# Performance work log

Hardware: AMD Instinct MI355X
Metric: run time of the kernel (lower is better)

## Reference

```python
import jax, jax.numpy as jnp
import numpy as np

B_SZ, L, H, P = 4, 4096, 1024, 1024
R_MIN, R_MAX, MAX_PHASE = 0.0, 1.0, 6.28


def setup_inputs() -> dict:
    key = jax.random.key(0)
    ks = jax.random.split(key, 8)
    inputs = jax.random.normal(ks[0], (B_SZ, L, H), dtype=jnp.float32)
    # LRU-style init for nu_log/theta_log (keeps |lambda| < 1 so scan is stable)
    u1 = jax.random.uniform(ks[1], (P,))
    nu = -0.5 * jnp.log(u1 * (R_MAX**2 - R_MIN**2) + R_MIN**2)
    nu_log = jnp.log(nu)
    u2 = jax.random.uniform(ks[2], (P,))
    theta_log = jnp.log(MAX_PHASE * u2)
    # variance_scaling(0.5,'fan_out','normal') for B; (1.0,'fan_out','normal') for C
    B_re = jax.random.normal(ks[3], (P, H)) * jnp.sqrt(0.5 / P)
    B_im = jax.random.normal(ks[4], (P, H)) * jnp.sqrt(0.5 / P)
    C_re = jax.random.normal(ks[5], (H, P)) * jnp.sqrt(1.0 / H)
    C_im = jax.random.normal(ks[6], (H, P)) * jnp.sqrt(1.0 / H)
    D = jax.random.normal(ks[7], (H,))
    diag_lambda = jnp.exp(-jnp.exp(nu_log) + 1j * jnp.exp(theta_log))
    gamma_log = jnp.log(jnp.sqrt(1.0 - jnp.abs(diag_lambda) ** 2))
    return {
        "inputs": inputs,
        "nu_log": nu_log.astype(jnp.float32),
        "theta_log": theta_log.astype(jnp.float32),
        "B_re": B_re.astype(jnp.float32),
        "B_im": B_im.astype(jnp.float32),
        "C_re": C_re.astype(jnp.float32),
        "C_im": C_im.astype(jnp.float32),
        "D": D.astype(jnp.float32),
        "gamma_log": gamma_log.astype(jnp.float32),
    }


def reference(inputs, nu_log, theta_log, B_re, B_im, C_re, C_im, D, gamma_log):
    batch_size, input_length, _ = inputs.shape
    Lambda = jnp.exp(-jnp.exp(nu_log) + 1j * jnp.exp(theta_log))  # [P] complex
    Bmat = B_re + 1j * B_im                                        # [P,H]
    Cmat = C_re + 1j * C_im                                        # [H,P]
    gamma = jnp.exp(gamma_log)                                     # [P]
    B_norm = Bmat * gamma[:, None]

    def apply_step(elem_i, elem_j):
        a_i, bu_i = elem_i
        a_j, bu_j = elem_j
        return (a_j * a_i, a_j * bu_i + bu_j)

    Ls = jnp.broadcast_to(Lambda, (batch_size, input_length, Lambda.shape[0]))
    Bu = jnp.einsum('ph,blh->blp', B_norm, inputs.astype(B_norm.dtype))
    _, xs = jax.lax.associative_scan(apply_step, (Ls, Bu), axis=1)
    Cx = jnp.einsum('hp,blp->blh', Cmat, xs).real
    Du = D * inputs
    return Cx + Du
```

## Files before the change

### kernel.cpp

```cpp
#include <hip/hip_runtime.h>
#include <cstdint>
#include <cstddef>

#define MDIM 16384
#define HDIM 1024
#define PDIM 1024
#define LSEQ 4096
#define BSZ  4
#define CHUNK 64
#define NCHUNK 64
#define NBU  2048

typedef float   floatx4  __attribute__((ext_vector_type(4)));
typedef __bf16  bf16x8   __attribute__((ext_vector_type(8)));
typedef unsigned short u16;
typedef unsigned short u16x8 __attribute__((ext_vector_type(8)));
typedef unsigned short u16x4 __attribute__((ext_vector_type(4)));

__device__ __forceinline__ u16 f2bf(float f) {
    union { float f; uint32_t u; } v; v.f = f;
    return (u16)((v.u + 0x7fffu + ((v.u >> 16) & 1u)) >> 16);
}
__device__ __forceinline__ float bfu2f(uint32_t bits16) {
    union { float f; uint32_t u; } v; v.u = bits16 << 16; return v.f;
}
__device__ __forceinline__ bf16x8 ldfrag(const u16* p) {
    return __builtin_bit_cast(bf16x8, *(const u16x8*)p);
}
__device__ __forceinline__ void gload16(const u16* g, u16* l) {
    __builtin_amdgcn_global_load_lds(
        (const __attribute__((address_space(1))) uint32_t*)g,
        (__attribute__((address_space(3))) uint32_t*)l, 16, 0, 0);
}

template<int KD>
__device__ __forceinline__ void gemm_core(
    const u16* __restrict__ A, const u16* __restrict__ B,
    int m0, int n0, u16* sA, u16* sB, floatx4 acc[4][4])
{
    const int tid  = threadIdx.x;
    const int wave = tid >> 6, lane = tid & 63;
    const int lrow = lane & 15, lq = lane >> 4;
    const int wm = (wave >> 1) * 64, wn = (wave & 1) * 64;
    const int srow   = lane >> 3;
    const int schunk = (lane & 7) ^ srow;

    const u16* aptr = A + (size_t)(m0 + wave * 32 + srow) * KD + schunk * 8;
    const u16* bptr = B + (size_t)(n0 + wave * 32 + srow) * KD + schunk * 8;
    u16* sAw = sA + wave * 32 * 64;
    u16* sBw = sB + wave * 32 * 64;

    for (int k0 = 0; k0 < KD; k0 += 64) {
        #pragma unroll
        for (int i = 0; i < 4; ++i) {
            gload16(aptr + (size_t)i * 8 * KD + k0, sAw + i * 8 * 64);
            gload16(bptr + (size_t)i * 8 * KD + k0, sBw + i * 8 * 64);
        }
        __syncthreads();
        #pragma unroll
        for (int s = 0; s < 2; ++s) {
            bf16x8 af[4], bfr[4];
            #pragma unroll
            for (int mt = 0; mt < 4; ++mt) {
                int r = wm + mt * 16 + lrow;
                af[mt] = ldfrag(sA + r * 64 + (((s * 4 + lq) ^ (r & 7)) * 8));
            }
            #pragma unroll
            for (int nt = 0; nt < 4; ++nt) {
                int r = wn + nt * 16 + lrow;
                bfr[nt] = ldfrag(sB + r * 64 + (((s * 4 + lq) ^ (r & 7)) * 8));
            }
            #pragma unroll
            for (int mt = 0; mt < 4; ++mt)
                #pragma unroll
                for (int nt = 0; nt < 4; ++nt)
                    acc[mt][nt] = __builtin_amdgcn_mfma_f32_16x16x32_bf16(
                        af[mt], bfr[nt], acc[mt][nt], 0, 0, 0);
        }
        __syncthreads();
    }
}

__global__ __launch_bounds__(256) void gemm_bu_k(
    const u16* __restrict__ A, const u16* __restrict__ B, u16* __restrict__ O)
{
    __shared__ u16 sA[128 * 64];
    __shared__ u16 sB[128 * 64];
    floatx4 acc[4][4] = {};
    const int m0 = blockIdx.x * 128, n0 = blockIdx.y * 128;
    gemm_core<HDIM>(A, B, m0, n0, sA, sB, acc);

    const int tid = threadIdx.x, wave = tid >> 6, lane = tid & 63;
    const int lrow = lane & 15, lq = lane >> 4;
    const int wm = (wave >> 1) * 64, wn = (wave & 1) * 64;
    #pragma unroll
    for (int nt = 0; nt < 4; ++nt) {
        int col = n0 + wn + nt * 16 + lrow;
        #pragma unroll
        for (int mt = 0; mt < 4; ++mt)
            #pragma unroll
            for (int r = 0; r < 4; ++r) {
                int row = m0 + wm + mt * 16 + lq * 4 + r;
                O[(size_t)row * NBU + col] = f2bf(acc[mt][nt][r]);
            }
    }
}

__global__ __launch_bounds__(256) void gemm_out_k(
    const u16* __restrict__ A, const u16* __restrict__ B,
    const float* __restrict__ Dv, const u16* __restrict__ Ubf,
    float* __restrict__ O)
{
    __shared__ u16 sA[128 * 64];
    __shared__ u16 sB[128 * 64];
    floatx4 acc[4][4] = {};
    const int m0 = blockIdx.x * 128, n0 = blockIdx.y * 128;
    gemm_core<NBU>(A, B, m0, n0, sA, sB, acc);

    const int tid = threadIdx.x, wave = tid >> 6, lane = tid & 63;
    const int lrow = lane & 15, lq = lane >> 4;
    const int wm = (wave >> 1) * 64, wn = (wave & 1) * 64;
    #pragma unroll
    for (int nt = 0; nt < 4; ++nt) {
        int col = n0 + wn + nt * 16 + lrow;
        float d = Dv[col];
        #pragma unroll
        for (int mt = 0; mt < 4; ++mt)
            #pragma unroll
            for (int r = 0; r < 4; ++r) {
                int row = m0 + wm + mt * 16 + lq * 4 + r;
                size_t o = (size_t)row * HDIM + col;
                O[o] = acc[mt][nt][r] + d * bfu2f(Ubf[o]);
            }
    }
}

__global__ __launch_bounds__(256) void cvt_u_bf(
    const float* __restrict__ in, u16* __restrict__ out)
{
    size_t i = ((size_t)blockIdx.x * 256 + threadIdx.x) * 8;
    float4 a = *(const float4*)(in + i);
    float4 b = *(const float4*)(in + i + 4);
    u16x8 w;
    w[0]=f2bf(a.x); w[1]=f2bf(a.y); w[2]=f2bf(a.z); w[3]=f2bf(a.w);
    w[4]=f2bf(b.x); w[5]=f2bf(b.y); w[6]=f2bf(b.z); w[7]=f2bf(b.w);
    *(u16x8*)(out + i) = w;
}

__global__ __launch_bounds__(256) void prep_bcomb(
    const float* __restrict__ Bre, const float* __restrict__ Bim,
    const float* __restrict__ gamma_log, u16* __restrict__ out)
{
    int t = blockIdx.x * 256 + threadIdx.x;
    int n = t >> 7;
    int h = (t & 127) * 8;
    int p = n >> 1, s = n & 1;
    const float* src = (s ? Bim : Bre) + (size_t)p * HDIM + h;
    float g = expf(gamma_log[p]);
    float4 a = *(const float4*)src;
    float4 b = *(const float4*)(src + 4);
    u16x8 w;
    w[0]=f2bf(a.x*g); w[1]=f2bf(a.y*g); w[2]=f2bf(a.z*g); w[3]=f2bf(a.w*g);
    w[4]=f2bf(b.x*g); w[5]=f2bf(b.y*g); w[6]=f2bf(b.z*g); w[7]=f2bf(b.w*g);
    *(u16x8*)(out + (size_t)n * HDIM + h) = w;
}

__global__ __launch_bounds__(256) void prep_bc(
    const float* __restrict__ Cre, const float* __restrict__ Cim,
    u16* __restrict__ out)
{
    int t = blockIdx.x * 256 + threadIdx.x;
    int h = t >> 8;
    int k = (t & 255) * 4;
    float4 cr = *(const float4*)(Cre + (size_t)h * PDIM + k);
    float4 ci = *(const float4*)(Cim + (size_t)h * PDIM + k);
    u16x8 w;
    w[0]=f2bf(cr.x); w[1]=f2bf(-ci.x);
    w[2]=f2bf(cr.y); w[3]=f2bf(-ci.y);
    w[4]=f2bf(cr.z); w[5]=f2bf(-ci.z);
    w[6]=f2bf(cr.w); w[7]=f2bf(-ci.w);
    *(u16x8*)(out + (size_t)h * NBU + 2 * k) = w;
}

__global__ __launch_bounds__(256) void scan_passA(
    const uint32_t* __restrict__ BuC,
    const float* __restrict__ nu_log, const float* __restrict__ theta_log,
    float* __restrict__ endC)
{
    int tid = blockIdx.x * 256 + threadIdx.x;
    int p = tid & (PDIM - 1);
    int c = (tid >> 10) & (NCHUNK - 1);
    int b = tid >> 16;
    float nu = expf(nu_log[p]);
    float th = expf(theta_log[p]);
    float el = expf(-nu);
    float lr = el * cosf(th), li = el * sinf(th);
    const uint32_t* src = BuC + (size_t)(b * LSEQ + c * CHUNK) * PDIM + p;
    float xr = 0.f, xi = 0.f;
    #pragma unroll 8
    for (int t = 0; t < CHUNK; ++t) {
        uint32_t v = src[(size_t)t * PDIM];
        float br = bfu2f(v & 0xffffu), bi = bfu2f(v >> 16);
        float nr = fmaf(lr, xr, fmaf(-li, xi, br));
        float ni = fmaf(lr, xi, fmaf(li, xr, bi));
        xr = nr; xi = ni;
    }
    float2 e; e.x = xr; e.y = xi;
    *(float2*)(endC + (size_t)tid * 2) = e;
}

__global__ __launch_bounds__(256) void scan_passB(
    const float* __restrict__ endC,
    const float* __restrict__ nu_log, const float* __restrict__ theta_log,
    float* __restrict__ carryC)
{
    int tid = blockIdx.x * 256 + threadIdx.x;
    int p = tid & (PDIM - 1);
    int b = tid >> 10;
    float nu = expf(nu_log[p]);
    float th = expf(theta_log[p]);
    float e64 = expf(-nu * (float)CHUNK);
    float a = th * (float)CHUNK;
    float Lr = e64 * cosf(a), Li = e64 * sinf(a);
    float gr = 0.f, gi = 0.f;
    for (int c = 0; c < NCHUNK; ++c) {
        size_t idx = (((size_t)b * NCHUNK + c) * PDIM + p) * 2;
        float2 g; g.x = gr; g.y = gi;
        *(float2*)(carryC + idx) = g;
        float2 e = *(const float2*)(endC + idx);
        float nr = fmaf(Lr, gr, fmaf(-Li, gi, e.x));
        float ni = fmaf(Lr, gi, fmaf(Li, gr, e.y));
        gr = nr; gi = ni;
    }
}

__global__ __launch_bounds__(256) void scan_passC(
    uint32_t* __restrict__ BuC,
    const float* __restrict__ nu_log, const float* __restrict__ theta_log,
    const float* __restrict__ carryC)
{
    int tid = blockIdx.x * 256 + threadIdx.x;
    int p = tid & (PDIM - 1);
    int c = (tid >> 10) & (NCHUNK - 1);
    int b = tid >> 16;
    float nu = expf(nu_log[p]);
    float th = expf(theta_log[p]);
    float el = expf(-nu);
    float lr = el * cosf(th), li = el * sinf(th);
    float2 g = *(const float2*)(carryC + (size_t)tid * 2);
    float xr = g.x, xi = g.y;
    uint32_t* ptr = BuC + (size_t)(b * LSEQ + c * CHUNK) * PDIM + p;
    #pragma unroll 8
    for (int t = 0; t < CHUNK; ++t) {
        uint32_t v = ptr[(size_t)t * PDIM];
        float br = bfu2f(v & 0xffffu), bi = bfu2f(v >> 16);
        float nr = fmaf(lr, xr, fmaf(-li, xi, br));
        float ni = fmaf(lr, xi, fmaf(li, xr, bi));
        xr = nr; xi = ni;
        ptr[(size_t)t * PDIM] = (uint32_t)f2bf(xr) | ((uint32_t)f2bf(xi) << 16);
    }
}

extern "C" void kernel_launch(void* const* d_in, const int* in_sizes, int n_in,
                              void* d_out, int out_size, void* d_ws, size_t ws_size,
                              hipStream_t stream)
{
    (void)in_sizes; (void)n_in; (void)out_size; (void)ws_size;
    const float* U         = (const float*)d_in[0];
    const float* nu_log    = (const float*)d_in[1];
    const float* theta_log = (const float*)d_in[2];
    const float* B_re      = (const float*)d_in[3];
    const float* B_im      = (const float*)d_in[4];
    const float* C_re      = (const float*)d_in[5];
    const float* C_im      = (const float*)d_in[6];
    const float* Dv        = (const float*)d_in[7];
    const float* gamma_log = (const float*)d_in[8];
    float* out = (float*)d_out;

    char* ws = (char*)d_ws;
    u16*      BuC    = (u16*)ws;
    u16*      Ubf    = (u16*)(ws + (size_t)64 * 1024 * 1024);
    u16*      Bcomb  = (u16*)(ws + (size_t)96 * 1024 * 1024);
    u16*      Bcbf   = (u16*)(ws + (size_t)100 * 1024 * 1024);
    float*    endC   = (float*)(ws + (size_t)104 * 1024 * 1024);
    float*    carryC = (float*)(ws + (size_t)106 * 1024 * 1024);

    cvt_u_bf <<<(MDIM * HDIM) / (256 * 8), 256, 0, stream>>>(U, Ubf);
    prep_bcomb<<<(NBU * HDIM) / (256 * 8), 256, 0, stream>>>(B_re, B_im, gamma_log, Bcomb);
    prep_bc  <<<(HDIM * PDIM) / (256 * 4), 256, 0, stream>>>(C_re, C_im, Bcbf);

    dim3 g1(MDIM / 128, NBU / 128);
    gemm_bu_k<<<g1, 256, 0, stream>>>(Ubf, Bcomb, BuC);

    const int nscan = BSZ * NCHUNK * PDIM;
    scan_passA<<<nscan / 256, 256, 0, stream>>>((const uint32_t*)BuC, nu_log, theta_log, endC);
    scan_passB<<<(BSZ * PDIM) / 256, 256, 0, stream>>>(endC, nu_log, theta_log, carryC);
    scan_passC<<<nscan / 256, 256, 0, stream>>>((uint32_t*)BuC, nu_log, theta_log, carryC);

    dim3 g3(MDIM / 128, HDIM / 128);
    gemm_out_k<<<g3, 256, 0, stream>>>(BuC, Bcbf, Dv, Ubf, out);
}
```

Before: 359.5 us.

## Stage GEMM output through LDS, swap grid order, and process two states per scan thread

The Bu GEMM epilogue now writes the bf16 tile to padded shared memory and stores it to global memory in 16-byte coalesced rows, replacing scattered 2-byte stores. Both GEMMs swap grid axes so consecutive blocks walk along N, which changes L2 reuse of the A tiles. All three scan passes handle two adjacent P states per thread with wider vector loads and stores, and pass B batches its endC loads eight at a time for more memory-level parallelism. The cost is half as many threads in the scan passes, which lowers the parallelism available for the sequential recurrences.

```diff
diff --git a/kernel.cpp b/kernel.cpp
--- a/kernel.cpp
+++ b/kernel.cpp
@@ -15,7 +15,6 @@
 typedef __bf16  bf16x8   __attribute__((ext_vector_type(8)));
 typedef unsigned short u16;
 typedef unsigned short u16x8 __attribute__((ext_vector_type(8)));
-typedef unsigned short u16x4 __attribute__((ext_vector_type(4)));
 
 __device__ __forceinline__ u16 f2bf(float f) {
     union { float f; uint32_t u; } v; v.f = f;
@@ -81,28 +80,41 @@
     }
 }
 
+#define ST 136
 __global__ __launch_bounds__(256) void gemm_bu_k(
     const u16* __restrict__ A, const u16* __restrict__ B, u16* __restrict__ O)
 {
-    __shared__ u16 sA[128 * 64];
-    __shared__ u16 sB[128 * 64];
+    __shared__ u16 smem[128 * ST];
+    u16* sA = smem;
+    u16* sB = smem + 128 * 64;
     floatx4 acc[4][4] = {};
-    const int m0 = blockIdx.x * 128, n0 = blockIdx.y * 128;
+    const int n0 = blockIdx.x * 128, m0 = blockIdx.y * 128;
     gemm_core<HDIM>(A, B, m0, n0, sA, sB, acc);
 
     const int tid = threadIdx.x, wave = tid >> 6, lane = tid & 63;
     const int lrow = lane & 15, lq = lane >> 4;
     const int wm = (wave >> 1) * 64, wn = (wave & 1) * 64;
+
     #pragma unroll
     for (int nt = 0; nt < 4; ++nt) {
-        int col = n0 + wn + nt * 16 + lrow;
+        int col = wn + nt * 16 + lrow;
         #pragma unroll
         for (int mt = 0; mt < 4; ++mt)
             #pragma unroll
             for (int r = 0; r < 4; ++r) {
-                int row = m0 + wm + mt * 16 + lq * 4 + r;
-                O[(size_t)row * NBU + col] = f2bf(acc[mt][nt][r]);
+                int row = wm + mt * 16 + lq * 4 + r;
+                smem[row * ST + col] = f2bf(acc[mt][nt][r]);
             }
+    }
+    __syncthreads();
+
+    const int col = (tid & 15) * 8;
+    const int rb  = tid >> 4;
+    #pragma unroll
+    for (int j = 0; j < 8; ++j) {
+        int row = rb + j * 16;
+        *(u16x8*)(O + (size_t)(m0 + row) * NBU + n0 + col) =
+            *(const u16x8*)(smem + row * ST + col);
     }
 }
 
@@ -114,7 +126,7 @@
     __shared__ u16 sA[128 * 64];
     __shared__ u16 sB[128 * 64];
     floatx4 acc[4][4] = {};
-    const int m0 = blockIdx.x * 128, n0 = blockIdx.y * 128;
+    const int n0 = blockIdx.x * 128, m0 = blockIdx.y * 128;
     gemm_core<NBU>(A, B, m0, n0, sA, sB, acc);
 
     const int tid = threadIdx.x, wave = tid >> 6, lane = tid & 63;
@@ -188,25 +200,29 @@
     float* __restrict__ endC)
 {
     int tid = blockIdx.x * 256 + threadIdx.x;
-    int p = tid & (PDIM - 1);
-    int c = (tid >> 10) & (NCHUNK - 1);
-    int b = tid >> 16;
-    float nu = expf(nu_log[p]);
-    float th = expf(theta_log[p]);
-    float el = expf(-nu);
-    float lr = el * cosf(th), li = el * sinf(th);
-    const uint32_t* src = BuC + (size_t)(b * LSEQ + c * CHUNK) * PDIM + p;
-    float xr = 0.f, xi = 0.f;
+    int p0 = (tid & 511) * 2;
+    int c  = (tid >> 9) & (NCHUNK - 1);
+    int b  = tid >> 15;
+    float nu0 = expf(nu_log[p0]),     th0 = expf(theta_log[p0]);
+    float nu1 = expf(nu_log[p0 + 1]), th1 = expf(theta_log[p0 + 1]);
+    float el0 = expf(-nu0), el1 = expf(-nu1);
+    float lr0 = el0 * cosf(th0), li0 = el0 * sinf(th0);
+    float lr1 = el1 * cosf(th1), li1 = el1 * sinf(th1);
+    const uint32_t* src = BuC + (size_t)(b * LSEQ + c * CHUNK) * PDIM + p0;
+    float xr0 = 0.f, xi0 = 0.f, xr1 = 0.f, xi1 = 0.f;
     #pragma unroll 8
     for (int t = 0; t < CHUNK; ++t) {
-        uint32_t v = src[(size_t)t * PDIM];
-        float br = bfu2f(v & 0xffffu), bi = bfu2f(v >> 16);
-        float nr = fmaf(lr, xr, fmaf(-li, xi, br));
-        float ni = fmaf(lr, xi, fmaf(li, xr, bi));
-        xr = nr; xi = ni;
-    }
-    float2 e; e.x = xr; e.y = xi;
-    *(float2*)(endC + (size_t)tid * 2) = e;
+        uint2 v = *(const uint2*)(src + (size_t)t * PDIM);
+        float br0 = bfu2f(v.x & 0xffffu), bi0 = bfu2f(v.x >> 16);
+        float br1 = bfu2f(v.y & 0xffffu), bi1 = bfu2f(v.y >> 16);
+        float nr0 = fmaf(lr0, xr0, fmaf(-li0, xi0, br0));
+        float ni0 = fmaf(lr0, xi0, fmaf(li0, xr0, bi0));
+        float nr1 = fmaf(lr1, xr1, fmaf(-li1, xi1, br1));
+        float ni1 = fmaf(lr1, xi1, fmaf(li1, xr1, bi1));
+        xr0 = nr0; xi0 = ni0; xr1 = nr1; xi1 = ni1;
+    }
+    float4 e; e.x = xr0; e.y = xi0; e.z = xr1; e.w = xi1;
+    *(float4*)(endC + (((size_t)b * NCHUNK + c) * PDIM + p0) * 2) = e;
 }
 
 __global__ __launch_bounds__(256) void scan_passB(
@@ -215,22 +231,31 @@
     float* __restrict__ carryC)
 {
     int tid = blockIdx.x * 256 + threadIdx.x;
-    int p = tid & (PDIM - 1);
-    int b = tid >> 10;
-    float nu = expf(nu_log[p]);
-    float th = expf(theta_log[p]);
-    float e64 = expf(-nu * (float)CHUNK);
-    float a = th * (float)CHUNK;
-    float Lr = e64 * cosf(a), Li = e64 * sinf(a);
-    float gr = 0.f, gi = 0.f;
-    for (int c = 0; c < NCHUNK; ++c) {
-        size_t idx = (((size_t)b * NCHUNK + c) * PDIM + p) * 2;
-        float2 g; g.x = gr; g.y = gi;
-        *(float2*)(carryC + idx) = g;
-        float2 e = *(const float2*)(endC + idx);
-        float nr = fmaf(Lr, gr, fmaf(-Li, gi, e.x));
-        float ni = fmaf(Lr, gi, fmaf(Li, gr, e.y));
-        gr = nr; gi = ni;
+    int p0 = (tid & 511) * 2;
+    int b  = tid >> 9;
+    float nu0 = expf(nu_log[p0]),     th0 = expf(theta_log[p0]);
+    float nu1 = expf(nu_log[p0 + 1]), th1 = expf(theta_log[p0 + 1]);
+    float e0 = expf(-nu0 * (float)CHUNK), a0 = th0 * (float)CHUNK;
+    float e1 = expf(-nu1 * (float)CHUNK), a1 = th1 * (float)CHUNK;
+    float Lr0 = e0 * cosf(a0), Li0 = e0 * sinf(a0);
+    float Lr1 = e1 * cosf(a1), Li1 = e1 * sinf(a1);
+    float gr0 = 0.f, gi0 = 0.f, gr1 = 0.f, gi1 = 0.f;
+    for (int g = 0; g < 8; ++g) {
+        float4 e[8];
+        #pragma unroll
+        for (int j = 0; j < 8; ++j)
+            e[j] = *(const float4*)(endC + (((size_t)b * NCHUNK + g * 8 + j) * PDIM + p0) * 2);
+        #pragma unroll
+        for (int j = 0; j < 8; ++j) {
+            size_t idx = (((size_t)b * NCHUNK + g * 8 + j) * PDIM + p0) * 2;
+            float4 go; go.x = gr0; go.y = gi0; go.z = gr1; go.w = gi1;
+            *(float4*)(carryC + idx) = go;
+            float nr0 = fmaf(Lr0, gr0, fmaf(-Li0, gi0, e[j].x));
+            float ni0 = fmaf(Lr0, gi0, fmaf(Li0, gr0, e[j].y));
+            float nr1 = fmaf(Lr1, gr1, fmaf(-Li1, gi1, e[j].z));
+            float ni1 = fmaf(Lr1, gi1, fmaf(Li1, gr1, e[j].w));
+            gr0 = nr0; gi0 = ni0; gr1 = nr1; gi1 = ni1;
+        }
     }
 }
 
@@ -240,24 +265,32 @@
     const float* __restrict__ carryC)
 {
     int tid = blockIdx.x * 256 + threadIdx.x;
-    int p = tid & (PDIM - 1);
-    int c = (tid >> 10) & (NCHUNK - 1);
-    int b = tid >> 16;
-    float nu = expf(nu_log[p]);
-    float th = expf(theta_log[p]);
-    float el = expf(-nu);
-    float lr = el * cosf(th), li = el * sinf(th);
-    float2 g = *(const float2*)(carryC + (size_t)tid * 2);
-    float xr = g.x, xi = g.y;
-    uint32_t* ptr = BuC + (size_t)(b * LSEQ + c * CHUNK) * PDIM + p;
+    int p0 = (tid & 511) * 2;
+    int c  = (tid >> 9) & (NCHUNK - 1);
+    int b  = tid >> 15;
+    float nu0 = expf(nu_log[p0]),     th0 = expf(theta_log[p0]);
+    float nu1 = expf(nu_log[p0 + 1]), th1 = expf(theta_log[p0 + 1]);
+    float el0 = expf(-nu0), el1 = expf(-nu1);
+    float lr0 = el0 * cosf(th0), li0 = el0 * sinf(th0);
+    float lr1 = el1 * cosf(th1), li1 = el1 * sinf(th1);
+    float4 g = *(const float4*)(carryC + (((size_t)b * NCHUNK + c) * PDIM + p0) * 2);
+    float xr0 = g.x, xi0 = g.y, xr1 = g.z, xi1 = g.w;
+    uint32_t* ptr = BuC + (size_t)(b * LSEQ + c * CHUNK) * PDIM + p0;
     #pragma unroll 8
     for (int t = 0; t < CHUNK; ++t) {
-        uint32_t v = ptr[(size_t)t * PDIM];
-        float br = bfu2f(v & 0xffffu), bi = bfu2f(v >> 16);
-        float nr = fmaf(lr, xr, fmaf(-li, xi, br));
-        float ni = fmaf(lr, xi, fmaf(li, xr, bi));
-        xr = nr; xi = ni;
-        ptr[(size_t)t * PDIM] = (uint32_t)f2bf(xr) | ((uint32_t)f2bf(xi) << 16);
+        uint32_t* q = ptr + (size_t)t * PDIM;
+        uint2 v = *(const uint2*)q;
+        float br0 = bfu2f(v.x & 0xffffu), bi0 = bfu2f(v.x >> 16);
+        float br1 = bfu2f(v.y & 0xffffu), bi1 = bfu2f(v.y >> 16);
+        float nr0 = fmaf(lr0, xr0, fmaf(-li0, xi0, br0));
+        float ni0 = fmaf(lr0, xi0, fmaf(li0, xr0, bi0));
+        float nr1 = fmaf(lr1, xr1, fmaf(-li1, xi1, br1));
+        float ni1 = fmaf(lr1, xi1, fmaf(li1, xr1, bi1));
+        xr0 = nr0; xi0 = ni0; xr1 = nr1; xi1 = ni1;
+        uint2 o;
+        o.x = (uint32_t)f2bf(xr0) | ((uint32_t)f2bf(xi0) << 16);
+        o.y = (uint32_t)f2bf(xr1) | ((uint32_t)f2bf(xi1) << 16);
+        *(uint2*)q = o;
     }
 }
 
@@ -278,25 +311,26 @@
     float* out = (float*)d_out;
 
     char* ws = (char*)d_ws;
-    u16*      BuC    = (u16*)ws;
-    u16*      Ubf    = (u16*)(ws + (size_t)64 * 1024 * 1024);
-    u16*      Bcomb  = (u16*)(ws + (size_t)96 * 1024 * 1024);
-    u16*      Bcbf   = (u16*)(ws + (size_t)100 * 1024 * 1024);
-    float*    endC   = (float*)(ws + (size_t)104 * 1024 * 1024);
-    float*    carryC = (float*)(ws + (size_t)106 * 1024 * 1024);
-
-    cvt_u_bf <<<(MDIM * HDIM) / (256 * 8), 256, 0, stream>>>(U, Ubf);
+    u16*   BuC    = (u16*)ws;
+    u16*   Ubf    = (u16*)(ws + (size_t)64 * 1024 * 1024);
+    u16*   Bcomb  = (u16*)(ws + (size_t)96 * 1024 * 1024);
+    u16*   Bcbf   = (u16*)(ws + (size_t)100 * 1024 * 1024);
+    float* endC   = (float*)(ws + (size_t)104 * 1024 * 1024);
+    float* carryC = (float*)(ws + (size_t)106 * 1024 * 1024);
+
+    cvt_u_bf  <<<(MDIM * HDIM) / (256 * 8), 256, 0, stream>>>(U, Ubf);
     prep_bcomb<<<(NBU * HDIM) / (256 * 8), 256, 0, stream>>>(B_re, B_im, gamma_log, Bcomb);
-    prep_bc  <<<(HDIM * PDIM) / (256 * 4), 256, 0, stream>>>(C_re, C_im, Bcbf);
-
-    dim3 g1(MDIM / 128, NBU / 128);
+    prep_bc   <<<(HDIM * PDIM) / (256 * 4), 256, 0, stream>>>(C_re, C_im, Bcbf);
+
+    dim3 g1(NBU / 128, MDIM / 128);
     gemm_bu_k<<<g1, 256, 0, stream>>>(Ubf, Bcomb, BuC);
 
-    const int nscan = BSZ * NCHUNK * PDIM;
-    scan_passA<<<nscan / 256, 256, 0, stream>>>((const uint32_t*)BuC, nu_log, theta_log, endC);
-    scan_passB<<<(BSZ * PDIM) / 256, 256, 0, stream>>>(endC, nu_log, theta_log, carryC);
-    scan_passC<<<nscan / 256, 256, 0, stream>>>((uint32_t*)BuC, nu_log, theta_log, carryC);
-
-    dim3 g3(MDIM / 128, HDIM / 128);
+    scan_passA<<<(BSZ * NCHUNK * PDIM / 2) / 256, 256, 0, stream>>>(
+        (const uint32_t*)BuC, nu_log, theta_log, endC);
+    scan_passB<<<(BSZ * PDIM / 2) / 256, 256, 0, stream>>>(endC, nu_log, theta_log, carryC);
+    scan_passC<<<(BSZ * NCHUNK * PDIM / 2) / 256, 256, 0, stream>>>(
+        (uint32_t*)BuC, nu_log, theta_log, carryC);
+
+    dim3 g3(HDIM / 128, MDIM / 128);
     gemm_out_k<<<g3, 256, 0, stream>>>(BuC, Bcbf, Dv, Ubf, out);
 }
```

Measured after the change: 357.0 us. Within noise of the previous version (-0.7%).
